# Kernel optimization log

Measured on AMD Instinct MI355X. Metric: run time of the kernel, lower is better.

## Reference

```python
import jax, jax.numpy as jnp
import numpy as np

NUM_HEADS = 4
HEAD_DIM = 64
IN_CH = 192
KERNEL_SIZES = (3, 5, 7, 9)  # per-head neighborhood size
NEG_INF = -1e30


def setup_inputs() -> dict:
    key = jax.random.key(0)
    k1, k2, k3 = jax.random.split(key, 3)
    x = jax.random.normal(k1, (8, IN_CH, 96, 96), dtype=jnp.float32)
    # QKV conv: out_channels = head_dim * num_heads * 3 = 768, 3x3, pad 1
    w_qkv = jax.random.normal(k2, (HEAD_DIM * NUM_HEADS * 3, IN_CH, 3, 3), dtype=jnp.float32) * 0.02
    b_qkv = jax.random.normal(k3, (HEAD_DIM * NUM_HEADS * 3,), dtype=jnp.float32) * 0.02
    return {"x": x, "w_qkv": w_qkv, "b_qkv": b_qkv}


def _neighborhood_attention(q, k, v, ksize):
    # q, k, v: [N, H, W, D]; KxK zero-padded neighborhood attention with
    # out-of-bounds positions masked out.
    N, H, W, D = q.shape
    pad = ksize // 2
    kp = jnp.pad(k, ((0, 0), (pad, pad), (pad, pad), (0, 0)))
    vp = jnp.pad(v, ((0, 0), (pad, pad), (pad, pad), (0, 0)))
    scale = 1.0 / np.sqrt(D).astype(np.float32)
    rows = jnp.arange(H)
    cols = jnp.arange(W)
    scores, masks = [], []
    for di in range(ksize):
        for dj in range(ksize):
            k_sh = kp[:, di:di + H, dj:dj + W, :]           # shifted keys
            scores.append(jnp.einsum('nhwd,nhwd->nhw', q, k_sh))
            rv = (rows + di - pad >= 0) & (rows + di - pad < H)   # [H]
            cv = (cols + dj - pad >= 0) & (cols + dj - pad < W)   # [W]
            masks.append(rv[:, None] & cv[None, :])               # [H, W]
    scores = jnp.stack(scores, axis=-1) * scale                   # [N,H,W,K2]
    mask = jnp.stack(masks, axis=-1)[None]                        # [1,H,W,K2]
    scores = jnp.where(mask, scores, NEG_INF)
    attn = jax.nn.softmax(scores, axis=-1)                        # [N,H,W,K2]
    out = jnp.zeros_like(q)
    t = 0
    for di in range(ksize):
        for dj in range(ksize):
            out = out + attn[..., t, None] * vp[:, di:di + H, dj:dj + W, :]
            t += 1
    return out  # [N,H,W,D]


def reference(x, w_qkv, b_qkv):
    # Dense QKV projection (Conv2d, stride 1, padding 1 == SAME for k=3)
    qkv = jax.lax.conv_general_dilated(
        x, w_qkv, window_strides=(1, 1), padding='SAME',
        dimension_numbers=('NCHW', 'OIHW', 'NCHW'))
    qkv = qkv + b_qkv[None, :, None, None]
    # transform_to_nhw1c: NCHW -> NHWC, then split channels into
    # num_heads blocks of 3*head_dim, each split into q, k, v.
    N, C, H, W = qkv.shape
    qkv = jnp.transpose(qkv, (0, 2, 3, 1)).reshape(N, H, W, NUM_HEADS, 3, HEAD_DIM)
    outs = []
    for h, ks in enumerate(KERNEL_SIZES):
        q = qkv[..., h, 0, :]
        k = qkv[..., h, 1, :]
        v = qkv[..., h, 2, :]
        o = _neighborhood_attention(q, k, v, ks)       # [N,H,W,D]
        outs.append(jnp.transpose(o, (0, 3, 1, 2)))    # transform_from_nhw1c -> NCHW
    return jnp.stack(outs, axis=0)  # [num_heads, N, D, H, W]
```

## Files before the change

kernel.cpp:

```cpp
#include <hip/hip_runtime.h>
#include <hip/hip_bf16.h>

#define NH 96
#define NW 96
#define NB 8
#define CIN 192
#define COUT 768
#define PH 98

typedef __attribute__((ext_vector_type(8))) unsigned short ushort8;
typedef __attribute__((ext_vector_type(8))) short bf16x8;
typedef __attribute__((ext_vector_type(4))) float f32x4;

static __device__ __forceinline__ unsigned short f2bf(float f) {
    unsigned int u = __float_as_uint(f);
    return (unsigned short)((u + 0x7fffu + ((u >> 16) & 1u)) >> 16);
}

typedef const __attribute__((address_space(1))) unsigned int gu32;
typedef __attribute__((address_space(3))) unsigned int lu32;
static __device__ __forceinline__ void gload16(const void* g, void* l) {
    __builtin_amdgcn_global_load_lds((gu32*)g, (lu32*)l, 16, 0, 0);
}

__global__ __launch_bounds__(256) void pack_x_kernel(
    const float* __restrict__ x, unsigned short* __restrict__ xp)
{
    __shared__ float tile[32][97];
    int bid = blockIdx.x;
    int ct = bid % 6; int y = (bid / 6) % NH; int n = bid / (6 * NH);
    int tid = threadIdx.x;
    int c0 = ct * 32;
    for (int i = tid; i < 32 * 96; i += 256) {
        int c = i / 96, xx = i % 96;
        tile[c][xx] = x[(((size_t)n * CIN + c0 + c) * NH + y) * NW + xx];
    }
    __syncthreads();
    for (int i = tid; i < 96 * 4; i += 256) {
        int xx = i >> 2, ch = i & 3;
        ushort8 pk;
#pragma unroll
        for (int j = 0; j < 8; ++j) pk[j] = f2bf(tile[ch * 8 + j][xx]);
        *(ushort8*)(xp + ((size_t)(n * PH + y + 1) * PH + xx + 1) * CIN + c0 + ch * 8) = pk;
    }
}

__global__ __launch_bounds__(256) void pack_w_kernel(
    const float* __restrict__ w, unsigned short* __restrict__ bw)
{
    __shared__ float ls[1728];
    int co = blockIdx.x; int tid = threadIdx.x;
    for (int i = tid; i < 1728; i += 256) ls[i] = w[(size_t)co * 1728 + i];
    __syncthreads();
    for (int i = tid; i < 1728; i += 256) {
        int sh = i / 192, ci = i % 192;
        bw[(size_t)co * 1728 + i] = f2bf(ls[ci * 9 + sh]);
    }
}

#define BUFSZ 24576

#define STAGE(S, BUF)                                                          \
    {                                                                          \
        int shift_ = (S) / 6, kk_ = (S) - shift_ * 6;                          \
        int aO_ = ((shift_ / 3) * PH + (shift_ % 3)) * CIN + kk_ * 32;         \
        int bO_ = (S) * 32;                                                    \
        gload16(srcA[0] + aO_, dstA[0] + (BUF));                               \
        gload16(srcA[1] + aO_, dstA[1] + (BUF));                               \
        _Pragma("unroll")                                                      \
        for (int i_ = 0; i_ < 4; ++i_)                                         \
            gload16(srcB[i_] + bO_, dstB[i_] + (BUF));                         \
    }

#define COMPUTE(CUR)                                                           \
    {                                                                          \
        bf16x8 af[8], bf[4];                                                   \
        _Pragma("unroll")                                                      \
        for (int m_ = 0; m_ < 8; ++m_)                                         \
            af[m_] = *(const bf16x8*)(smem + (CUR) + aoff[m_]);                \
        _Pragma("unroll")                                                      \
        for (int n_ = 0; n_ < 4; ++n_)                                         \
            bf[n_] = *(const bf16x8*)(smem + (CUR) + boff[n_]);                \
        __builtin_amdgcn_s_setprio(1);                                         \
        _Pragma("unroll")                                                      \
        for (int m_ = 0; m_ < 8; ++m_)                                         \
            _Pragma("unroll")                                                  \
            for (int n_ = 0; n_ < 4; ++n_)                                     \
                acc[m_][n_] = __builtin_amdgcn_mfma_f32_16x16x32_bf16(         \
                    af[m_], bf[n_], acc[m_][n_], 0, 0, 0);                     \
        __builtin_amdgcn_s_setprio(0);                                         \
    }

__global__ __launch_bounds__(256, 2) void conv_gemm_kernel(
    const unsigned short* __restrict__ xp, const unsigned short* __restrict__ bw,
    const float* __restrict__ bias, unsigned short* __restrict__ qkq,
    unsigned short* __restrict__ vt)
{
    __shared__ __align__(16) char smem[3 * BUFSZ];
    int bid = (blockIdx.x & 7) * 216 + (blockIdx.x >> 3);
    int brow = (bid / 3) * 128, bcol = (bid % 3) * 256;
    int tid = threadIdx.x, lane = tid & 63, wn = tid >> 6;

    const unsigned short* srcA[2];
    const unsigned short* srcB[4];
    char* dstA[2];
    char* dstB[4];
#pragma unroll
    for (int i = 0; i < 2; ++i) {
        int s = i * 256 + tid;
        int row = s >> 2, c = s & 3;
        int p = brow + row;
        int n = p / 9216; int rem = p - n * 9216;
        int y = rem / 96; int xx = rem - y * 96;
        int csw = (c ^ ((row >> 1) & 3)) << 3;
        srcA[i] = xp + ((size_t)(n * PH + y) * PH + xx) * CIN + csw;
        dstA[i] = smem + (i * 256 + (tid & ~63)) * 16;
    }
#pragma unroll
    for (int i = 0; i < 4; ++i) {
        int s = i * 256 + tid;
        int row = s >> 2, c = s & 3;
        int csw = (c ^ ((row >> 1) & 3)) << 3;
        srcB[i] = bw + (size_t)(bcol + row) * 1728 + csw;
        dstB[i] = smem + 8192 + (i * 256 + (tid & ~63)) * 16;
    }

    int aoff[8], boff[4];
#pragma unroll
    for (int m = 0; m < 8; ++m) {
        int rowA = m * 16 + (lane & 15);
        aoff[m] = rowA * 64 + (((lane >> 4) ^ ((rowA >> 1) & 3)) << 4);
    }
#pragma unroll
    for (int n = 0; n < 4; ++n) {
        int colB = wn * 64 + n * 16 + (lane & 15);
        boff[n] = 8192 + colB * 64 + (((lane >> 4) ^ ((colB >> 1) & 3)) << 4);
    }

    STAGE(0, 0);
    STAGE(1, BUFSZ);

    f32x4 acc[8][4] = {};

    for (int t = 0; t < 52; ++t) {
        asm volatile("s_waitcnt vmcnt(6)" ::: "memory");
        __builtin_amdgcn_s_barrier();
        STAGE(t + 2, ((t + 2) % 3) * BUFSZ);
        __builtin_amdgcn_sched_barrier(0);
        COMPUTE((t % 3) * BUFSZ);
    }
    asm volatile("s_waitcnt vmcnt(6)" ::: "memory");
    __builtin_amdgcn_s_barrier();
    COMPUTE((52 % 3) * BUFSZ);
    asm volatile("s_waitcnt vmcnt(0)" ::: "memory");
    __builtin_amdgcn_s_barrier();
    COMPUTE((53 % 3) * BUFSZ);

    __syncthreads();
    unsigned short* sc = (unsigned short*)smem;
    float bn[4];
#pragma unroll
    for (int n = 0; n < 4; ++n)
        bn[n] = bias[bcol + wn * 64 + n * 16 + (lane & 15)];
#pragma unroll
    for (int m = 0; m < 8; ++m)
#pragma unroll
        for (int n = 0; n < 4; ++n) {
            int col = wn * 64 + n * 16 + (lane & 15);
            int cabs = bcol + col;
            float scale = ((cabs % 192) < 64) ? 0.125f : 1.0f;
#pragma unroll
            for (int j = 0; j < 4; ++j) {
                int row = m * 16 + (lane >> 4) * 4 + j;
                sc[row * 256 + (col ^ ((row & 7) << 3))] =
                    f2bf((acc[m][n][j] + bn[n]) * scale);
            }
        }
    __syncthreads();
#pragma unroll
    for (int i = 0; i < 16; ++i) {
        int idx = i * 256 + tid;
        int row = idx >> 5, ch = idx & 31;
        int c0 = bcol + ch * 8;
        int r192 = c0 % 192;
        if (r192 < 128) {
            ushort8 pk = *(const ushort8*)(sc + row * 256 + ((ch * 8) ^ ((row & 7) << 3)));
            *(ushort8*)(qkq + (size_t)(brow + row) * 512 + (c0 / 192) * 128 + r192) = pk;
        }
    }
    int nblk = brow / 9216;
    int prem = brow - nblk * 9216;
#pragma unroll
    for (int h = 0; h < 4; ++h) {
        int lc = h * 192 + 128 - bcol;
        if (lc < 0 || lc > 192) continue;
        unsigned short* vth = vt + (size_t)h * 4718592;
#pragma unroll
        for (int it = 0; it < 4; ++it) {
            int i = it * 256 + tid;
            int d = i & 63, pxb = i >> 6;
            ushort8 pk;
#pragma unroll
            for (int j = 0; j < 8; ++j) {
                int px = pxb * 8 + j;
                pk[j] = sc[px * 256 + ((lc + d) ^ ((px & 7) << 3))];
            }
            *(ushort8*)(vth + ((size_t)(nblk * 64 + d)) * 9216 + prem + pxb * 8) = pk;
        }
    }
}

#define SLAB 24576
template<int KS>
static __device__ __forceinline__ void na_body(
    const unsigned short* __restrict__ qkq, const unsigned short* __restrict__ vt,
    float* __restrict__ out, int head, int bid, char* nsm)
{
    constexpr int PAD = KS / 2;
    float (*sO)[97] = (float(*)[97])nsm;
    int y = bid % 96, n = bid / 96;
    int tid = threadIdx.x;
    int wv = tid >> 6, lane = tid & 63;
    int g = lane >> 4, pix = lane & 15;
    int x0 = wv * 16;
    int x = x0 + pix;
    int W = x0 - 8;

    size_t qbase = ((size_t)((n * 96 + y) * 96 + x)) * 512 + (size_t)head * 128;
    bf16x8 qf0 = *(const bf16x8*)(qkq + qbase + g * 8);
    bf16x8 qf1 = *(const bf16x8*)(qkq + qbase + 32 + g * 8);
    asm volatile("s_waitcnt vmcnt(0)" ::: "memory");

    const size_t hoff = (size_t)head * 128 + 64;
#define STAGEKV(DI, BUF)                                                       \
    {                                                                          \
        int iy_ = min(max(y + (DI) - PAD, 0), 95);                             \
        size_t rb_ = ((size_t)((n * 96 + iy_) * 96)) * 512 + hoff;             \
        _Pragma("unroll")                                                      \
        for (int i_ = 0; i_ < 2; ++i_) {                                       \
            int ch_ = i_ * 384 + tid;                                          \
            int xx_ = ch_ >> 3, c8_ = (ch_ & 7) ^ (xx_ & 7);                   \
            gload16(qkq + rb_ + (size_t)xx_ * 512 + c8_ * 8,                   \
                    nsm + (BUF) * SLAB + (i_ * 384 + (tid & ~63)) * 16);       \
        }                                                                      \
        _Pragma("unroll")                                                      \
        for (int i_ = 0; i_ < 2; ++i_) {                                       \
            int ch_ = i_ * 384 + tid;                                          \
            int d_ = ch_ / 12, c_ = ch_ % 12;                                  \
            int cs_ = c_ ^ ((d_ >> 1) & 3);                                    \
            gload16(vt + (((size_t)(n * 64 + d_) * 96 + iy_)) * 96 + cs_ * 8,  \
                    nsm + (BUF) * SLAB + 12288 + (i_ * 384 + (tid & ~63)) * 16); \
        }                                                                      \
    }

    STAGEKV(0, 0);
    STAGEKV(1, 1);

    float l = 0.f;
    f32x4 O[4] = {};
    int addrA = ((2 * (g & 1)) * 16 + pix) * 4;
    int addrB = addrA + 64;
    bool kthi = (g >> 1) != 0;
    int cxg = min(max(2 * wv - 1 + g, 0), 11);
    int vbase = 12288 + pix * 192 + ((cxg ^ ((pix >> 1) & 3)) << 4);

#pragma unroll
    for (int di = 0; di < KS; ++di) {
        if (di < KS - 1) asm volatile("s_waitcnt vmcnt(4)" ::: "memory");
        else             asm volatile("s_waitcnt vmcnt(0)" ::: "memory");
        __builtin_amdgcn_s_barrier();
        __builtin_amdgcn_sched_barrier(0);
        if (di + 2 < KS) STAGEKV(di + 2, (di + 2) % 3);
        int iy = y + di - PAD;
        if (iy < 0 || iy >= 96) continue;
        const char* kb = nsm + (di % 3) * SLAB;

        f32x4 t[2];
#pragma unroll
        for (int kt = 0; kt < 2; ++kt) {
            int kix_l = W + kt * 16 + pix;
            int ixc = min(max(kix_l, 0), 95);
            const char* kr = kb + ixc * 128;
            bf16x8 kf0 = *(const bf16x8*)(kr + ((g ^ (ixc & 7)) << 4));
            bf16x8 kf1 = *(const bf16x8*)(kr + (((4 + g) ^ (ixc & 7)) << 4));
            f32x4 tt = {};
            tt = __builtin_amdgcn_mfma_f32_16x16x32_bf16(kf0, qf0, tt, 0, 0, 0);
            tt = __builtin_amdgcn_mfma_f32_16x16x32_bf16(kf1, qf1, tt, 0, 0, 0);
            t[kt] = tt;
        }

        unsigned int w0[2], w1[2];
#pragma unroll
        for (int kt = 0; kt < 2; ++kt) {
            float p[4];
#pragma unroll
            for (int r = 0; r < 4; ++r) {
                int kix = W + kt * 16 + g * 4 + r;
                bool valid = ((unsigned)(kix - x + PAD) <= (unsigned)(2 * PAD)) &&
                             ((unsigned)kix < 96u);
                p[r] = valid ? __expf(t[kt][r]) : 0.f;
            }
            l += (p[0] + p[1]) + (p[2] + p[3]);
            asm("v_cvt_pk_bf16_f32 %0, %1, %2" : "=v"(w0[kt]) : "v"(p[0]), "v"(p[1]));
            asm("v_cvt_pk_bf16_f32 %0, %1, %2" : "=v"(w1[kt]) : "v"(p[2]), "v"(p[3]));
        }
        int a0 = __builtin_amdgcn_ds_bpermute(addrA, (int)w0[0]);
        int b0 = __builtin_amdgcn_ds_bpermute(addrA, (int)w0[1]);
        int a1 = __builtin_amdgcn_ds_bpermute(addrA, (int)w1[0]);
        int b1 = __builtin_amdgcn_ds_bpermute(addrA, (int)w1[1]);
        int a2 = __builtin_amdgcn_ds_bpermute(addrB, (int)w0[0]);
        int b2 = __builtin_amdgcn_ds_bpermute(addrB, (int)w0[1]);
        int a3 = __builtin_amdgcn_ds_bpermute(addrB, (int)w1[0]);
        int b3 = __builtin_amdgcn_ds_bpermute(addrB, (int)w1[1]);
        union { int u[4]; bf16x8 v; } pa;
        pa.u[0] = kthi ? b0 : a0;
        pa.u[1] = kthi ? b1 : a1;
        pa.u[2] = kthi ? b2 : a2;
        pa.u[3] = kthi ? b3 : a3;

#pragma unroll
        for (int dc = 0; dc < 4; ++dc) {
            bf16x8 vf = *(const bf16x8*)(kb + dc * 3072 + vbase);
            O[dc] = __builtin_amdgcn_mfma_f32_16x16x32_bf16(pa.v, vf, O[dc], 0, 0, 0);
        }
    }

    l += __shfl_xor(l, 16, 64);
    l += __shfl_xor(l, 32, 64);
    float linv = 1.0f / l;
    float linvj[4];
#pragma unroll
    for (int j = 0; j < 4; ++j)
        linvj[j] = __uint_as_float((unsigned)__builtin_amdgcn_ds_bpermute(
            (4 * g + j) * 4, (int)__float_as_uint(linv)));
    __syncthreads();
#pragma unroll
    for (int dc = 0; dc < 4; ++dc)
#pragma unroll
        for (int j = 0; j < 4; ++j)
            sO[dc * 16 + pix][x0 + g * 4 + j] = O[dc][j] * linvj[j];
    __syncthreads();
    for (int i = tid; i < 1536; i += 384) {
        int d = i / 24, xq = i % 24;
        float4 v4 = { sO[d][xq * 4], sO[d][xq * 4 + 1],
                      sO[d][xq * 4 + 2], sO[d][xq * 4 + 3] };
        *(float4*)(out + ((size_t)(head * 8 + n) * 64 + d) * 9216
                   + y * 96 + xq * 4) = v4;
    }
}

__global__ __launch_bounds__(384, 3) void na_mfma_all(
    const unsigned short* __restrict__ qkq, const unsigned short* __restrict__ vt,
    float* __restrict__ out)
{
    __shared__ __align__(16) char nsm[3 * SLAB];
    int head = blockIdx.x & 3;
    int bid = blockIdx.x >> 2;
    switch (head) {
        case 0: na_body<3>(qkq, vt,               out, 0, bid, nsm); break;
        case 1: na_body<5>(qkq, vt + 4718592,     out, 1, bid, nsm); break;
        case 2: na_body<7>(qkq, vt + 2 * 4718592, out, 2, bid, nsm); break;
        default: na_body<9>(qkq, vt + 3 * 4718592, out, 3, bid, nsm); break;
    }
}

extern "C" void kernel_launch(void* const* d_in, const int* in_sizes, int n_in,
                              void* d_out, int out_size, void* d_ws, size_t ws_size,
                              hipStream_t stream) {
    const float* x  = (const float*)d_in[0];
    const float* w  = (const float*)d_in[1];
    const float* b  = (const float*)d_in[2];
    float* out = (float*)d_out;

    unsigned short* qkq  = (unsigned short*)d_ws;
    unsigned short* vt   = (unsigned short*)((char*)d_ws + 75497472);
    unsigned short* xpad = (unsigned short*)((char*)d_ws + 113246208);
    unsigned short* bw   = (unsigned short*)((char*)d_ws + 142749696);

    hipMemsetAsync(xpad, 0, 29503488, stream);
    pack_x_kernel<<<NB * NH * 6, 256, 0, stream>>>(x, xpad);
    pack_w_kernel<<<COUT, 256, 0, stream>>>(w, bw);
    conv_gemm_kernel<<<1728, 256, 0, stream>>>(xpad, bw, b, qkq, vt);

    na_mfma_all<<<4 * 768, 384, 0, stream>>>(qkq, vt, out);
}
```

Baseline: 343.3 us.

## Process two output rows per block to reuse staged K/V neighborhood rows

Each neighborhood-attention block now computes two adjacent output rows, staging KS+1 K/V rows instead of KS per row. Each staged row serves both output rows, which roughly halves global-to-LDS K/V traffic and fragment loads per output row. The grid is halved, accumulators and Q fragments are doubled, and launch bounds drop from 3 to 2 blocks per CU. The extra register pressure and lower occupancy may cut into the gain. The attention kernel is only part of the total time, alongside the conv GEMM.

```diff
diff --git a/kernel.cpp b/kernel.cpp
--- a/kernel.cpp
+++ b/kernel.cpp
@@ -217,8 +217,8 @@
     float* __restrict__ out, int head, int bid, char* nsm)
 {
     constexpr int PAD = KS / 2;
-    float (*sO)[97] = (float(*)[97])nsm;
-    int y = bid % 96, n = bid / 96;
+    int yp = bid % 48, n = bid / 48;
+    int y0 = yp * 2;
     int tid = threadIdx.x;
     int wv = tid >> 6, lane = tid & 63;
     int g = lane >> 4, pix = lane & 15;
@@ -226,15 +226,18 @@
     int x = x0 + pix;
     int W = x0 - 8;
 
-    size_t qbase = ((size_t)((n * 96 + y) * 96 + x)) * 512 + (size_t)head * 128;
-    bf16x8 qf0 = *(const bf16x8*)(qkq + qbase + g * 8);
-    bf16x8 qf1 = *(const bf16x8*)(qkq + qbase + 32 + g * 8);
+    size_t qb0 = ((size_t)((n * 96 + y0) * 96 + x)) * 512 + (size_t)head * 128;
+    size_t qb1 = qb0 + 96 * 512;
+    bf16x8 qa0 = *(const bf16x8*)(qkq + qb0 + g * 8);
+    bf16x8 qa1 = *(const bf16x8*)(qkq + qb0 + 32 + g * 8);
+    bf16x8 qc0 = *(const bf16x8*)(qkq + qb1 + g * 8);
+    bf16x8 qc1 = *(const bf16x8*)(qkq + qb1 + 32 + g * 8);
     asm volatile("s_waitcnt vmcnt(0)" ::: "memory");
 
     const size_t hoff = (size_t)head * 128 + 64;
 #define STAGEKV(DI, BUF)                                                       \
     {                                                                          \
-        int iy_ = min(max(y + (DI) - PAD, 0), 95);                             \
+        int iy_ = min(max(y0 + (DI) - PAD, 0), 95);                            \
         size_t rb_ = ((size_t)((n * 96 + iy_) * 96)) * 512 + hoff;             \
         _Pragma("unroll")                                                      \
         for (int i_ = 0; i_ < 2; ++i_) {                                       \
@@ -256,100 +259,115 @@
     STAGEKV(0, 0);
     STAGEKV(1, 1);
 
-    float l = 0.f;
-    f32x4 O[4] = {};
+    float l0 = 0.f, l1 = 0.f;
+    f32x4 O0[4] = {}, O1[4] = {};
     int addrA = ((2 * (g & 1)) * 16 + pix) * 4;
     int addrB = addrA + 64;
     bool kthi = (g >> 1) != 0;
     int cxg = min(max(2 * wv - 1 + g, 0), 11);
     int vbase = 12288 + pix * 192 + ((cxg ^ ((pix >> 1) & 3)) << 4);
 
-#pragma unroll
-    for (int di = 0; di < KS; ++di) {
-        if (di < KS - 1) asm volatile("s_waitcnt vmcnt(4)" ::: "memory");
-        else             asm volatile("s_waitcnt vmcnt(0)" ::: "memory");
+#define ROWCOMP(QF0, QF1, L, O)                                                \
+    {                                                                          \
+        unsigned int w0[2], w1[2];                                             \
+        _Pragma("unroll")                                                      \
+        for (int kt = 0; kt < 2; ++kt) {                                       \
+            f32x4 tt = {};                                                     \
+            tt = __builtin_amdgcn_mfma_f32_16x16x32_bf16(kf0[kt], QF0, tt, 0, 0, 0); \
+            tt = __builtin_amdgcn_mfma_f32_16x16x32_bf16(kf1[kt], QF1, tt, 0, 0, 0); \
+            float p[4];                                                        \
+            _Pragma("unroll")                                                  \
+            for (int r = 0; r < 4; ++r) {                                      \
+                int kix = W + kt * 16 + g * 4 + r;                             \
+                bool valid = ((unsigned)(kix - x + PAD) <= (unsigned)(2 * PAD)) && \
+                             ((unsigned)kix < 96u);                            \
+                p[r] = valid ? __expf(tt[r]) : 0.f;                            \
+            }                                                                  \
+            L += (p[0] + p[1]) + (p[2] + p[3]);                                \
+            asm("v_cvt_pk_bf16_f32 %0, %1, %2" : "=v"(w0[kt]) : "v"(p[0]), "v"(p[1])); \
+            asm("v_cvt_pk_bf16_f32 %0, %1, %2" : "=v"(w1[kt]) : "v"(p[2]), "v"(p[3])); \
+        }                                                                      \
+        int a0 = __builtin_amdgcn_ds_bpermute(addrA, (int)w0[0]);              \
+        int b0 = __builtin_amdgcn_ds_bpermute(addrA, (int)w0[1]);              \
+        int a1 = __builtin_amdgcn_ds_bpermute(addrA, (int)w1[0]);              \
+        int b1 = __builtin_amdgcn_ds_bpermute(addrA, (int)w1[1]);              \
+        int a2 = __builtin_amdgcn_ds_bpermute(addrB, (int)w0[0]);              \
+        int b2 = __builtin_amdgcn_ds_bpermute(addrB, (int)w0[1]);              \
+        int a3 = __builtin_amdgcn_ds_bpermute(addrB, (int)w1[0]);              \
+        int b3 = __builtin_amdgcn_ds_bpermute(addrB, (int)w1[1]);              \
+        union { int u[4]; bf16x8 v; } pa;                                      \
+        pa.u[0] = kthi ? b0 : a0;                                              \
+        pa.u[1] = kthi ? b1 : a1;                                              \
+        pa.u[2] = kthi ? b2 : a2;                                              \
+        pa.u[3] = kthi ? b3 : a3;                                              \
+        _Pragma("unroll")                                                      \
+        for (int dc = 0; dc < 4; ++dc)                                         \
+            O[dc] = __builtin_amdgcn_mfma_f32_16x16x32_bf16(pa.v, vf[dc], O[dc], 0, 0, 0); \
+    }
+
+#pragma unroll
+    for (int di = 0; di <= KS; ++di) {
+        if (di < KS) asm volatile("s_waitcnt vmcnt(4)" ::: "memory");
+        else         asm volatile("s_waitcnt vmcnt(0)" ::: "memory");
         __builtin_amdgcn_s_barrier();
         __builtin_amdgcn_sched_barrier(0);
-        if (di + 2 < KS) STAGEKV(di + 2, (di + 2) % 3);
-        int iy = y + di - PAD;
+        if (di + 2 <= KS) STAGEKV(di + 2, (di + 2) % 3);
+        int iy = y0 + di - PAD;
         if (iy < 0 || iy >= 96) continue;
         const char* kb = nsm + (di % 3) * SLAB;
 
-        f32x4 t[2];
+        bf16x8 kf0[2], kf1[2];
 #pragma unroll
         for (int kt = 0; kt < 2; ++kt) {
             int kix_l = W + kt * 16 + pix;
             int ixc = min(max(kix_l, 0), 95);
             const char* kr = kb + ixc * 128;
-            bf16x8 kf0 = *(const bf16x8*)(kr + ((g ^ (ixc & 7)) << 4));
-            bf16x8 kf1 = *(const bf16x8*)(kr + (((4 + g) ^ (ixc & 7)) << 4));
-            f32x4 tt = {};
-            tt = __builtin_amdgcn_mfma_f32_16x16x32_bf16(kf0, qf0, tt, 0, 0, 0);
-            tt = __builtin_amdgcn_mfma_f32_16x16x32_bf16(kf1, qf1, tt, 0, 0, 0);
-            t[kt] = tt;
+            kf0[kt] = *(const bf16x8*)(kr + ((g ^ (ixc & 7)) << 4));
+            kf1[kt] = *(const bf16x8*)(kr + (((4 + g) ^ (ixc & 7)) << 4));
         }
-
-        unsigned int w0[2], w1[2];
-#pragma unroll
-        for (int kt = 0; kt < 2; ++kt) {
-            float p[4];
-#pragma unroll
-            for (int r = 0; r < 4; ++r) {
-                int kix = W + kt * 16 + g * 4 + r;
-                bool valid = ((unsigned)(kix - x + PAD) <= (unsigned)(2 * PAD)) &&
-                             ((unsigned)kix < 96u);
-                p[r] = valid ? __expf(t[kt][r]) : 0.f;
-            }
-            l += (p[0] + p[1]) + (p[2] + p[3]);
-            asm("v_cvt_pk_bf16_f32 %0, %1, %2" : "=v"(w0[kt]) : "v"(p[0]), "v"(p[1]));
-            asm("v_cvt_pk_bf16_f32 %0, %1, %2" : "=v"(w1[kt]) : "v"(p[2]), "v"(p[3]));
+        bf16x8 vf[4];
+#pragma unroll
+        for (int dc = 0; dc < 4; ++dc)
+            vf[dc] = *(const bf16x8*)(kb + dc * 3072 + vbase);
+
+        if (di < KS)  ROWCOMP(qa0, qa1, l0, O0);
+        if (di >= 1)  ROWCOMP(qc0, qc1, l1, O1);
+    }
+
+    l0 += __shfl_xor(l0, 16, 64); l0 += __shfl_xor(l0, 32, 64);
+    l1 += __shfl_xor(l1, 16, 64); l1 += __shfl_xor(l1, 32, 64);
+    float li0 = 1.0f / l0, li1 = 1.0f / l1;
+    float lj0[4], lj1[4];
+#pragma unroll
+    for (int j = 0; j < 4; ++j) {
+        lj0[j] = __uint_as_float((unsigned)__builtin_amdgcn_ds_bpermute(
+            (4 * g + j) * 4, (int)__float_as_uint(li0)));
+        lj1[j] = __uint_as_float((unsigned)__builtin_amdgcn_ds_bpermute(
+            (4 * g + j) * 4, (int)__float_as_uint(li1)));
+    }
+    __syncthreads();
+    float (*sO2)[64][97] = (float(*)[64][97])nsm;
+#pragma unroll
+    for (int dc = 0; dc < 4; ++dc)
+#pragma unroll
+        for (int j = 0; j < 4; ++j) {
+            sO2[0][dc * 16 + pix][x0 + g * 4 + j] = O0[dc][j] * lj0[j];
+            sO2[1][dc * 16 + pix][x0 + g * 4 + j] = O1[dc][j] * lj1[j];
         }
-        int a0 = __builtin_amdgcn_ds_bpermute(addrA, (int)w0[0]);
-        int b0 = __builtin_amdgcn_ds_bpermute(addrA, (int)w0[1]);
-        int a1 = __builtin_amdgcn_ds_bpermute(addrA, (int)w1[0]);
-        int b1 = __builtin_amdgcn_ds_bpermute(addrA, (int)w1[1]);
-        int a2 = __builtin_amdgcn_ds_bpermute(addrB, (int)w0[0]);
-        int b2 = __builtin_amdgcn_ds_bpermute(addrB, (int)w0[1]);
-        int a3 = __builtin_amdgcn_ds_bpermute(addrB, (int)w1[0]);
-        int b3 = __builtin_amdgcn_ds_bpermute(addrB, (int)w1[1]);
-        union { int u[4]; bf16x8 v; } pa;
-        pa.u[0] = kthi ? b0 : a0;
-        pa.u[1] = kthi ? b1 : a1;
-        pa.u[2] = kthi ? b2 : a2;
-        pa.u[3] = kthi ? b3 : a3;
-
-#pragma unroll
-        for (int dc = 0; dc < 4; ++dc) {
-            bf16x8 vf = *(const bf16x8*)(kb + dc * 3072 + vbase);
-            O[dc] = __builtin_amdgcn_mfma_f32_16x16x32_bf16(pa.v, vf, O[dc], 0, 0, 0);
-        }
-    }
-
-    l += __shfl_xor(l, 16, 64);
-    l += __shfl_xor(l, 32, 64);
-    float linv = 1.0f / l;
-    float linvj[4];
-#pragma unroll
-    for (int j = 0; j < 4; ++j)
-        linvj[j] = __uint_as_float((unsigned)__builtin_amdgcn_ds_bpermute(
-            (4 * g + j) * 4, (int)__float_as_uint(linv)));
-    __syncthreads();
-#pragma unroll
-    for (int dc = 0; dc < 4; ++dc)
-#pragma unroll
-        for (int j = 0; j < 4; ++j)
-            sO[dc * 16 + pix][x0 + g * 4 + j] = O[dc][j] * linvj[j];
-    __syncthreads();
-    for (int i = tid; i < 1536; i += 384) {
-        int d = i / 24, xq = i % 24;
-        float4 v4 = { sO[d][xq * 4], sO[d][xq * 4 + 1],
-                      sO[d][xq * 4 + 2], sO[d][xq * 4 + 3] };
+    __syncthreads();
+    for (int i = tid; i < 3072; i += 384) {
+        int r = i >> 11;
+        int rem = i - r * 1536;
+        r = i / 1536; rem = i - r * 1536;
+        int d = rem / 24, xq = rem % 24;
+        float4 v4 = { sO2[r][d][xq * 4], sO2[r][d][xq * 4 + 1],
+                      sO2[r][d][xq * 4 + 2], sO2[r][d][xq * 4 + 3] };
         *(float4*)(out + ((size_t)(head * 8 + n) * 64 + d) * 9216
-                   + y * 96 + xq * 4) = v4;
-    }
-}
-
-__global__ __launch_bounds__(384, 3) void na_mfma_all(
+                   + (y0 + r) * 96 + xq * 4) = v4;
+    }
+}
+
+__global__ __launch_bounds__(384, 2) void na_mfma_all(
     const unsigned short* __restrict__ qkq, const unsigned short* __restrict__ vt,
     float* __restrict__ out)
 {
@@ -382,5 +400,5 @@
     pack_w_kernel<<<COUT, 256, 0, stream>>>(w, bw);
     conv_gemm_kernel<<<1728, 256, 0, stream>>>(xpad, bw, b, qkq, vt);
 
-    na_mfma_all<<<4 * 768, 384, 0, stream>>>(qkq, vt, out);
-}
+    na_mfma_all<<<4 * 384, 384, 0, stream>>>(qkq, vt, out);
+}
```

After: 329.6 us. 4.0% less time.
